# Optimization experiments

Hardware: AMD Instinct MI355X
Metric: run time of the kernel (lower is better)

Reference implementation:

```python
import jax, jax.numpy as jnp
import numpy as np

N_QUBITS = 10
N_LAYERS = 4
BATCH = 4096


def _apply_1q_batched(state, gate, q):
    # state: [B, 2,2,...,2]; gate: [B, 2, 2] (per-sample angles)
    s = jnp.moveaxis(state, 1 + q, -1)
    s = jnp.einsum('b...i,bji->b...j', s, gate)
    return jnp.moveaxis(s, -1, 1 + q)


def _apply_1q(state, gate, q):
    # gate: [2, 2] shared across batch
    s = jnp.moveaxis(state, 1 + q, -1)
    s = jnp.einsum('b...i,ji->b...j', s, gate)
    return jnp.moveaxis(s, -1, 1 + q)


def _apply_cnot(state, c, t):
    # bring control axis to 1 and target axis to 2, flip target where control==1
    s = jnp.moveaxis(state, (1 + c, 1 + t), (1, 2))
    s = jnp.concatenate([s[:, :1], s[:, 1:, ::-1]], axis=1)
    return jnp.moveaxis(s, (1, 2), (1 + c, 1 + t))


def _ry_rz_gate(theta_y, theta_z):
    # RZ(theta_z) @ RY(theta_y), both scalars -> [2, 2] complex
    hy = theta_y * 0.5
    cy, sy = jnp.cos(hy), jnp.sin(hy)
    ry = jnp.stack([jnp.stack([cy, -sy]), jnp.stack([sy, cy])]).astype(jnp.complex64)
    hz = theta_z * 0.5
    ph = jnp.exp(1j * jnp.stack([-hz, hz]).astype(jnp.complex64))  # diag of RZ
    return ph[:, None] * ry


def setup_inputs() -> dict:
    key = jax.random.key(0)
    kx, kp = jax.random.split(key)
    x = jax.random.uniform(kx, (BATCH, N_QUBITS), dtype=jnp.float32,
                           minval=-np.pi, maxval=np.pi)
    params = 0.5 * jax.random.normal(kp, (N_LAYERS, 2 * N_QUBITS), dtype=jnp.float32)
    return {"x": x, "params": params}


def reference(x, params):
    B, n = x.shape
    L = params.shape[0]
    dim = 2 ** n
    # |0...0> for every sample
    state = jnp.zeros((B, dim), jnp.complex64).at[:, 0].set(1.0)
    state = state.reshape((B,) + (2,) * n)

    # data encoding: RY(x[b, q]) on qubit q, per-sample angles
    half = x * 0.5
    c, s = jnp.cos(half), jnp.sin(half)  # [B, n]
    for q in range(n):
        g = jnp.stack([jnp.stack([c[:, q], -s[:, q]], -1),
                       jnp.stack([s[:, q], c[:, q]], -1)], -2).astype(jnp.complex64)  # [B,2,2]
        state = _apply_1q_batched(state, g, q)

    # variational layers: RY then RZ (fused) per qubit, then CNOT ring
    for l in range(L):
        for q in range(n):
            state = _apply_1q(state, _ry_rz_gate(params[l, q], params[l, n + q]), q)
        for q in range(n):
            state = _apply_cnot(state, q, (q + 1) % n)

    # <Z_q> = sum over basis states of |amp|^2 * (+1 if bit_q==0 else -1)
    probs = jnp.abs(state.reshape(B, dim)) ** 2  # float32 [B, 2^n]
    idx = jnp.arange(dim)
    bits = (idx[None, :] >> (n - 1 - jnp.arange(n))[:, None]) & 1  # [n, 2^n]
    signs = (1.0 - 2.0 * bits).astype(probs.dtype)
    return jnp.einsum('bs,qs->bq', probs, signs)  # [B, n]
```

## Files before the change

### kernel.cpp

```cpp
#include <hip/hip_runtime.h>

#define NQ 10

#if __has_builtin(__builtin_amdgcn_permlane16_swap)
#define HAVE_PLSWAP 1
#endif

template<int M>
__device__ __forceinline__ float lx(float v) {
    if constexpr (M == 1)
        return __int_as_float(__builtin_amdgcn_mov_dpp(__float_as_int(v), 0xB1, 0xF, 0xF, true));
    else if constexpr (M == 2)
        return __int_as_float(__builtin_amdgcn_mov_dpp(__float_as_int(v), 0x4E, 0xF, 0xF, true));
    else if constexpr (M == 8)
        return __int_as_float(__builtin_amdgcn_mov_dpp(__float_as_int(v), 0x128, 0xF, 0xF, true));
    else if constexpr (M == 4 || M == 16)
        return __int_as_float(__builtin_amdgcn_ds_swizzle(__float_as_int(v), (M << 10) | 0x1F));
    else
        return __shfl_xor(v, M, 64);
}

template<int M>
__device__ __forceinline__ float2 lx2(float2 v) {
    return make_float2(lx<M>(v.x), lx<M>(v.y));
}

template<int M>
__device__ __forceinline__ void xch(float& a, float& b) {
#ifdef HAVE_PLSWAP
    if constexpr (M == 16) {
        auto r1 = __builtin_amdgcn_permlane16_swap(__float_as_uint(a), __float_as_uint(b), false, false);
        auto r2 = __builtin_amdgcn_permlane16_swap(r1[1], r1[0], false, false);
        a = __uint_as_float(r2[0]);
        b = __uint_as_float(r2[1]);
    } else {
        auto r1 = __builtin_amdgcn_permlane32_swap(__float_as_uint(a), __float_as_uint(b), false, false);
        auto r2 = __builtin_amdgcn_permlane32_swap(r1[1], r1[0], false, false);
        a = __uint_as_float(r2[0]);
        b = __uint_as_float(r2[1]);
    }
#else
    a = lx<M>(a);
    b = lx<M>(b);
#endif
}

__device__ __forceinline__ float2 cmul(float2 a, float2 b) {
    return make_float2(a.x * b.x - a.y * b.y, a.x * b.y + a.y * b.x);
}

__device__ __forceinline__ float2 bperm2(int addr, float2 v) {
    float2 r;
    r.x = __int_as_float(__builtin_amdgcn_ds_bpermute(addr, __float_as_int(v.x)));
    r.y = __int_as_float(__builtin_amdgcn_ds_bpermute(addr, __float_as_int(v.y)));
    return r;
}

template<int M>
__device__ __forceinline__ void ry_lane(float2 st[16], int lane, float c, float s) {
    const float cB = (lane & M) ? s : -s;
#pragma unroll
    for (int r = 0; r < 16; ++r) {
        float2 part = lx2<M>(st[r]);
        st[r].x = c * st[r].x + cB * part.x;
        st[r].y = c * st[r].y + cB * part.y;
    }
}

template<int M>
__device__ __forceinline__ void ry_lane_x(float2 st[16], int lane, float c, float s) {
    const float cB = (lane & M) ? s : -s;
#pragma unroll
    for (int r = 0; r < 16; r += 2) {
        float pax = st[r].x, pay = st[r].y, pbx = st[r + 1].x, pby = st[r + 1].y;
        xch<M>(pax, pbx);
        xch<M>(pay, pby);
        st[r].x     = c * st[r].x     + cB * pax;
        st[r].y     = c * st[r].y     + cB * pay;
        st[r + 1].x = c * st[r + 1].x + cB * pbx;
        st[r + 1].y = c * st[r + 1].y + cB * pby;
    }
}

template<int M>
__device__ __forceinline__ void ry_lane_r(float sr[16], int lane, float c, float s) {
    const float cB = (lane & M) ? s : -s;
#pragma unroll
    for (int r = 0; r < 16; ++r) {
        float part = lx<M>(sr[r]);
        sr[r] = c * sr[r] + cB * part;
    }
}

template<int M>
__device__ __forceinline__ void ry_lane_r_x(float sr[16], int lane, float c, float s) {
    const float cB = (lane & M) ? s : -s;
#pragma unroll
    for (int r = 0; r < 16; r += 2) {
        float pa = sr[r], pb = sr[r + 1];
        xch<M>(pa, pb);
        sr[r]     = c * sr[r]     + cB * pa;
        sr[r + 1] = c * sr[r + 1] + cB * pb;
    }
}

template<int RB>
__device__ __forceinline__ void ry_reg_r(float sr[16], float c, float s) {
#pragma unroll
    for (int r = 0; r < 16; ++r) {
        if (r & RB) continue;
        float a0 = sr[r], a1 = sr[r | RB];
        sr[r]      = c * a0 - s * a1;
        sr[r | RB] = s * a0 + c * a1;
    }
}

template<int RB>
__device__ __forceinline__ void ry_reg(float2 st[16], float c, float s) {
#pragma unroll
    for (int r = 0; r < 16; ++r) {
        if (r & RB) continue;
        float2 a0 = st[r], a1 = st[r | RB];
        st[r].x = c * a0.x - s * a1.x;
        st[r].y = c * a0.y - s * a1.y;
        st[r | RB].x = s * a0.x + c * a1.x;
        st[r | RB].y = s * a0.y + c * a1.y;
    }
}

template<int MC, int RB>
__device__ __forceinline__ void cnot_lane_reg(float2 st[16], int lane) {
    const bool sel = (lane & MC) != 0;
#pragma unroll
    for (int r = 0; r < 16; ++r) {
        if (r & RB) continue;
        float2 lo = st[r], hi = st[r | RB];
        st[r]      = sel ? hi : lo;
        st[r | RB] = sel ? lo : hi;
    }
}

template<int RC, int RT>
__device__ __forceinline__ void cnot_reg_reg(float2 st[16]) {
#pragma unroll
    for (int r = 0; r < 16; ++r) {
        if ((r & RC) && !(r & RT)) {
            float2 t = st[r];
            st[r] = st[r | RT];
            st[r | RT] = t;
        }
    }
}

__device__ __forceinline__ void cnot_q9_q0(float2 st[16]) {
#pragma unroll
    for (int i = 0; i < 4; ++i) {
        const int ra = 4 * i + 1, rb = 4 * i + 3;
        xch<32>(st[ra].x, st[rb].x);
        xch<32>(st[ra].y, st[rb].y);
    }
}

__device__ __forceinline__ float wht64(float v, int lane) {
    float t;
    t = lx<1>(v);  v = (lane & 1)  ? (t - v) : (v + t);
    t = lx<2>(v);  v = (lane & 2)  ? (t - v) : (v + t);
    t = lx<4>(v);  v = (lane & 4)  ? (t - v) : (v + t);
    t = lx<8>(v);  v = (lane & 8)  ? (t - v) : (v + t);
    t = lx<16>(v); v = (lane & 16) ? (t - v) : (v + t);
    t = lx<32>(v); v = (lane & 32) ? (t - v) : (v + t);
    return v;
}

__global__ __launch_bounds__(256)
void pqc_kernel(const float* __restrict__ x,
                const float* __restrict__ params,
                float* __restrict__ out, int B) {
    const int lane = threadIdx.x & 63;
    const int wave = threadIdx.x >> 6;
    const int b = blockIdx.x * 4 + wave;
    if (b >= B) return;

    const float* xb = x + (long)b * NQ;
    float c0,s0,c1,s1,c2,s2,c3,s3,c4,s4,c5,s5,c6,s6,c7,s7,c8,s8,c9,s9;
    __sincosf(0.5f * xb[0], &s0, &c0);
    __sincosf(0.5f * xb[1], &s1, &c1);
    __sincosf(0.5f * xb[2], &s2, &c2);
    __sincosf(0.5f * xb[3], &s3, &c3);
    __sincosf(0.5f * xb[4], &s4, &c4);
    __sincosf(0.5f * xb[5], &s5, &c5);
    __sincosf(0.5f * xb[6], &s6, &c6);
    __sincosf(0.5f * xb[7], &s7, &c7);
    __sincosf(0.5f * xb[8], &s8, &c8);
    __sincosf(0.5f * xb[9], &s9, &c9);
    float laneprod = ((lane & 32) ? s0 : c0) * ((lane & 16) ? s1 : c1)
                   * ((lane & 8)  ? s2 : c2) * ((lane & 4)  ? s3 : c3)
                   * ((lane & 2)  ? s4 : c4) * ((lane & 1)  ? s5 : c5);
    float Ar[4] = { c6 * c7, c6 * s7, s6 * c7, s6 * s7 };
    float Br[4] = { c8 * c9, c8 * s9, s8 * c9, s8 * s9 };
    Ar[0] *= laneprod; Ar[1] *= laneprod; Ar[2] *= laneprod; Ar[3] *= laneprod;

    float sr[16];
#pragma unroll
    for (int r = 0; r < 16; ++r) sr[r] = Ar[r >> 2] * Br[r & 3];

    const float* p0 = params;
    float c, s;
    __sincosf(0.5f * p0[0], &s, &c); ry_lane_r_x<32>(sr, lane, c, s);
    __sincosf(0.5f * p0[1], &s, &c); ry_lane_r_x<16>(sr, lane, c, s);
    __sincosf(0.5f * p0[2], &s, &c); ry_lane_r<8>(sr, lane, c, s);
    __sincosf(0.5f * p0[3], &s, &c); ry_lane_r<4>(sr, lane, c, s);
    __sincosf(0.5f * p0[4], &s, &c); ry_lane_r<2>(sr, lane, c, s);
    __sincosf(0.5f * p0[5], &s, &c); ry_lane_r<1>(sr, lane, c, s);
    __sincosf(0.5f * p0[6], &s, &c); ry_reg_r<8>(sr, c, s);
    __sincosf(0.5f * p0[7], &s, &c); ry_reg_r<4>(sr, c, s);
    __sincosf(0.5f * p0[8], &s, &c); ry_reg_r<2>(sr, c, s);
    __sincosf(0.5f * p0[9], &s, &c); ry_reg_r<1>(sr, c, s);

    float2 st[16];
    {
        float sz, cz;
        __sincosf(0.5f * p0[10], &sz, &cz);
        float2 PL = make_float2(cz, (lane & 32) ? sz : -sz);
        __sincosf(0.5f * p0[11], &sz, &cz);
        PL = cmul(PL, make_float2(cz, (lane & 16) ? sz : -sz));
        __sincosf(0.5f * p0[12], &sz, &cz);
        PL = cmul(PL, make_float2(cz, (lane & 8) ? sz : -sz));
        __sincosf(0.5f * p0[13], &sz, &cz);
        PL = cmul(PL, make_float2(cz, (lane & 4) ? sz : -sz));
        __sincosf(0.5f * p0[14], &sz, &cz);
        PL = cmul(PL, make_float2(cz, (lane & 2) ? sz : -sz));
        __sincosf(0.5f * p0[15], &sz, &cz);
        PL = cmul(PL, make_float2(cz, (lane & 1) ? sz : -sz));

        float z6s, z6c, z7s, z7c, z8s, z8c, z9s, z9c;
        __sincosf(0.5f * p0[16], &z6s, &z6c);
        __sincosf(0.5f * p0[17], &z7s, &z7c);
        __sincosf(0.5f * p0[18], &z8s, &z8c);
        __sincosf(0.5f * p0[19], &z9s, &z9c);
        float2 A[4], Bb[4];
        A[0] = cmul(make_float2(z6c, -z6s), make_float2(z7c, -z7s));
        A[1] = cmul(make_float2(z6c, -z6s), make_float2(z7c,  z7s));
        A[2] = cmul(make_float2(z6c,  z6s), make_float2(z7c, -z7s));
        A[3] = cmul(make_float2(z6c,  z6s), make_float2(z7c,  z7s));
        Bb[0] = cmul(make_float2(z8c, -z8s), make_float2(z9c, -z9s));
        Bb[1] = cmul(make_float2(z8c, -z8s), make_float2(z9c,  z9s));
        Bb[2] = cmul(make_float2(z8c,  z8s), make_float2(z9c, -z9s));
        Bb[3] = cmul(make_float2(z8c,  z8s), make_float2(z9c,  z9s));
        A[0] = cmul(A[0], PL); A[1] = cmul(A[1], PL);
        A[2] = cmul(A[2], PL); A[3] = cmul(A[3], PL);
#pragma unroll
        for (int r = 0; r < 16; ++r) {
            float2 t = make_float2(sr[r] * A[r >> 2].x, sr[r] * A[r >> 2].y);
            st[r] = cmul(t, Bb[r & 3]);
        }
    }

    {
        const int addr = ((lane ^ (lane >> 1)) & 63) << 2;
#pragma unroll
        for (int r = 0; r < 16; ++r) st[r] = bperm2(addr, st[r]);
        cnot_lane_reg<1, 8>(st, lane);
        cnot_reg_reg<8, 4>(st);
        cnot_reg_reg<4, 2>(st);
        cnot_reg_reg<2, 1>(st);
        cnot_q9_q0(st);
    }

#pragma unroll
    for (int l = 1; l < 4; ++l) {
        const float* pl = params + l * 2 * NQ;

        __sincosf(0.5f * pl[0], &s, &c); ry_lane_x<32>(st, lane, c, s);
        __sincosf(0.5f * pl[1], &s, &c); ry_lane_x<16>(st, lane, c, s);
        __sincosf(0.5f * pl[2], &s, &c); ry_lane<8>(st, lane, c, s);
        __sincosf(0.5f * pl[3], &s, &c); ry_lane<4>(st, lane, c, s);
        __sincosf(0.5f * pl[4], &s, &c); ry_lane<2>(st, lane, c, s);
        __sincosf(0.5f * pl[5], &s, &c); ry_lane<1>(st, lane, c, s);
        __sincosf(0.5f * pl[6], &s, &c); ry_reg<8>(st, c, s);
        __sincosf(0.5f * pl[7], &s, &c); ry_reg<4>(st, c, s);
        __sincosf(0.5f * pl[8], &s, &c); ry_reg<2>(st, c, s);
        __sincosf(0.5f * pl[9], &s, &c); ry_reg<1>(st, c, s);

        if (l < 3) {
            float sz, cz;
            __sincosf(0.5f * pl[10], &sz, &cz);
            float2 PL = make_float2(cz, (lane & 32) ? sz : -sz);
            __sincosf(0.5f * pl[11], &sz, &cz);
            PL = cmul(PL, make_float2(cz, (lane & 16) ? sz : -sz));
            __sincosf(0.5f * pl[12], &sz, &cz);
            PL = cmul(PL, make_float2(cz, (lane & 8) ? sz : -sz));
            __sincosf(0.5f * pl[13], &sz, &cz);
            PL = cmul(PL, make_float2(cz, (lane & 4) ? sz : -sz));
            __sincosf(0.5f * pl[14], &sz, &cz);
            PL = cmul(PL, make_float2(cz, (lane & 2) ? sz : -sz));
            __sincosf(0.5f * pl[15], &sz, &cz);
            PL = cmul(PL, make_float2(cz, (lane & 1) ? sz : -sz));

            float z6s, z6c, z7s, z7c, z8s, z8c, z9s, z9c;
            __sincosf(0.5f * pl[16], &z6s, &z6c);
            __sincosf(0.5f * pl[17], &z7s, &z7c);
            __sincosf(0.5f * pl[18], &z8s, &z8c);
            __sincosf(0.5f * pl[19], &z9s, &z9c);
            float2 A[4], Bb[4];
            A[0] = cmul(make_float2(z6c, -z6s), make_float2(z7c, -z7s));
            A[1] = cmul(make_float2(z6c, -z6s), make_float2(z7c,  z7s));
            A[2] = cmul(make_float2(z6c,  z6s), make_float2(z7c, -z7s));
            A[3] = cmul(make_float2(z6c,  z6s), make_float2(z7c,  z7s));
            Bb[0] = cmul(make_float2(z8c, -z8s), make_float2(z9c, -z9s));
            Bb[1] = cmul(make_float2(z8c, -z8s), make_float2(z9c,  z9s));
            Bb[2] = cmul(make_float2(z8c,  z8s), make_float2(z9c, -z9s));
            Bb[3] = cmul(make_float2(z8c,  z8s), make_float2(z9c,  z9s));
            A[0] = cmul(A[0], PL); A[1] = cmul(A[1], PL);
            A[2] = cmul(A[2], PL); A[3] = cmul(A[3], PL);
#pragma unroll
            for (int r = 0; r < 16; ++r)
                st[r] = cmul(cmul(st[r], A[r >> 2]), Bb[r & 3]);

            const int addr = ((lane ^ (lane >> 1)) & 63) << 2;
#pragma unroll
            for (int r = 0; r < 16; ++r) st[r] = bperm2(addr, st[r]);
            cnot_lane_reg<1, 8>(st, lane);
            cnot_reg_reg<8, 4>(st);
            cnot_reg_reg<4, 2>(st);
            cnot_reg_reg<2, 1>(st);
            cnot_q9_q0(st);
        }
    }

    float lane_sum = 0.f, A3 = 0.f, A32 = 0.f, A321 = 0.f, A3210 = 0.f;
#pragma unroll
    for (int r = 0; r < 16; ++r) {
        float p = st[r].x * st[r].x + st[r].y * st[r].y;
        const int p3 = (r >> 3) & 1;
        const int p32 = p3 ^ ((r >> 2) & 1);
        const int p321 = p32 ^ ((r >> 1) & 1);
        const int p3210 = p321 ^ (r & 1);
        lane_sum += p;
        A3    += p3    ? -p : p;
        A32   += p32   ? -p : p;
        A321  += p321  ? -p : p;
        A3210 += p3210 ? -p : p;
    }
    const float wLS   = wht64(lane_sum, lane);
    const float w3    = wht64(A3, lane);
    const float w32   = wht64(A32, lane);
    const float w321  = wht64(A321, lane);
    const float w3210 = wht64(A3210, lane);

    const long base = (long)b * NQ;
    if (lane == 31) out[base + 0] = w3210;
    if (lane == 48) out[base + 1] = wLS;
    if (lane == 56) out[base + 2] = wLS;
    if (lane == 60) out[base + 3] = wLS;
    if (lane == 62) out[base + 4] = wLS;
    if (lane == 63) {
        out[base + 5] = wLS;
        out[base + 6] = w3;
        out[base + 7] = w32;
        out[base + 8] = w321;
        out[base + 9] = w3210;
    }
}

extern "C" void kernel_launch(void* const* d_in, const int* in_sizes, int n_in,
                              void* d_out, int out_size, void* d_ws, size_t ws_size,
                              hipStream_t stream) {
    const float* x = (const float*)d_in[0];
    const float* params = (const float*)d_in[1];
    float* out = (float*)d_out;
    const int B = in_sizes[0] / NQ;
    const int grid = (B + 3) / 4;
    pqc_kernel<<<grid, 256, 0, stream>>>(x, params, out, B);
}
```

Before: 87.61 us.

## Precompute gate trig tables in a setup kernel and read them from workspace

Adds a setup kernel that computes sincos of the encoding angles per sample and all parameter gate cos/sin, per-lane folded RZ diagonals and Bb factors into the workspace. The main kernel then loads these instead of recomputing transcendental functions in every wave. It also swaps the lane-xor-4 exchange from ds_swizzle to a two-DPP sequence. The cost is an extra kernel launch plus global memory round trips, and the old path is kept as a fallback when no workspace is available.

```diff
diff --git a/kernel.cpp b/kernel.cpp
--- a/kernel.cpp
+++ b/kernel.cpp
@@ -5,6 +5,11 @@
 #if __has_builtin(__builtin_amdgcn_permlane16_swap)
 #define HAVE_PLSWAP 1
 #endif
+
+constexpr int GATE_OFF = 0;
+constexpr int BB_OFF = 80;
+constexpr int AFOLD_OFF = 112;
+constexpr int ENC_OFF = 2048;
 
 template<int M>
 __device__ __forceinline__ float lx(float v) {
@@ -12,10 +17,13 @@
         return __int_as_float(__builtin_amdgcn_mov_dpp(__float_as_int(v), 0xB1, 0xF, 0xF, true));
     else if constexpr (M == 2)
         return __int_as_float(__builtin_amdgcn_mov_dpp(__float_as_int(v), 0x4E, 0xF, 0xF, true));
-    else if constexpr (M == 8)
+    else if constexpr (M == 4) {
+        int t = __builtin_amdgcn_mov_dpp(__float_as_int(v), 0x141, 0xF, 0xF, true);
+        return __int_as_float(__builtin_amdgcn_mov_dpp(t, 0x1B, 0xF, 0xF, true));
+    } else if constexpr (M == 8)
         return __int_as_float(__builtin_amdgcn_mov_dpp(__float_as_int(v), 0x128, 0xF, 0xF, true));
-    else if constexpr (M == 4 || M == 16)
-        return __int_as_float(__builtin_amdgcn_ds_swizzle(__float_as_int(v), (M << 10) | 0x1F));
+    else if constexpr (M == 16)
+        return __int_as_float(__builtin_amdgcn_ds_swizzle(__float_as_int(v), (16 << 10) | 0x1F));
     else
         return __shfl_xor(v, M, 64);
 }
@@ -173,116 +181,25 @@
 }
 
 __global__ __launch_bounds__(256)
-void pqc_kernel(const float* __restrict__ x,
-                const float* __restrict__ params,
-                float* __restrict__ out, int B) {
-    const int lane = threadIdx.x & 63;
-    const int wave = threadIdx.x >> 6;
-    const int b = blockIdx.x * 4 + wave;
-    if (b >= B) return;
-
-    const float* xb = x + (long)b * NQ;
-    float c0,s0,c1,s1,c2,s2,c3,s3,c4,s4,c5,s5,c6,s6,c7,s7,c8,s8,c9,s9;
-    __sincosf(0.5f * xb[0], &s0, &c0);
-    __sincosf(0.5f * xb[1], &s1, &c1);
-    __sincosf(0.5f * xb[2], &s2, &c2);
-    __sincosf(0.5f * xb[3], &s3, &c3);
-    __sincosf(0.5f * xb[4], &s4, &c4);
-    __sincosf(0.5f * xb[5], &s5, &c5);
-    __sincosf(0.5f * xb[6], &s6, &c6);
-    __sincosf(0.5f * xb[7], &s7, &c7);
-    __sincosf(0.5f * xb[8], &s8, &c8);
-    __sincosf(0.5f * xb[9], &s9, &c9);
-    float laneprod = ((lane & 32) ? s0 : c0) * ((lane & 16) ? s1 : c1)
-                   * ((lane & 8)  ? s2 : c2) * ((lane & 4)  ? s3 : c3)
-                   * ((lane & 2)  ? s4 : c4) * ((lane & 1)  ? s5 : c5);
-    float Ar[4] = { c6 * c7, c6 * s7, s6 * c7, s6 * s7 };
-    float Br[4] = { c8 * c9, c8 * s9, s8 * c9, s8 * s9 };
-    Ar[0] *= laneprod; Ar[1] *= laneprod; Ar[2] *= laneprod; Ar[3] *= laneprod;
-
-    float sr[16];
-#pragma unroll
-    for (int r = 0; r < 16; ++r) sr[r] = Ar[r >> 2] * Br[r & 3];
-
-    const float* p0 = params;
-    float c, s;
-    __sincosf(0.5f * p0[0], &s, &c); ry_lane_r_x<32>(sr, lane, c, s);
-    __sincosf(0.5f * p0[1], &s, &c); ry_lane_r_x<16>(sr, lane, c, s);
-    __sincosf(0.5f * p0[2], &s, &c); ry_lane_r<8>(sr, lane, c, s);
-    __sincosf(0.5f * p0[3], &s, &c); ry_lane_r<4>(sr, lane, c, s);
-    __sincosf(0.5f * p0[4], &s, &c); ry_lane_r<2>(sr, lane, c, s);
-    __sincosf(0.5f * p0[5], &s, &c); ry_lane_r<1>(sr, lane, c, s);
-    __sincosf(0.5f * p0[6], &s, &c); ry_reg_r<8>(sr, c, s);
-    __sincosf(0.5f * p0[7], &s, &c); ry_reg_r<4>(sr, c, s);
-    __sincosf(0.5f * p0[8], &s, &c); ry_reg_r<2>(sr, c, s);
-    __sincosf(0.5f * p0[9], &s, &c); ry_reg_r<1>(sr, c, s);
-
-    float2 st[16];
-    {
-        float sz, cz;
-        __sincosf(0.5f * p0[10], &sz, &cz);
-        float2 PL = make_float2(cz, (lane & 32) ? sz : -sz);
-        __sincosf(0.5f * p0[11], &sz, &cz);
-        PL = cmul(PL, make_float2(cz, (lane & 16) ? sz : -sz));
-        __sincosf(0.5f * p0[12], &sz, &cz);
-        PL = cmul(PL, make_float2(cz, (lane & 8) ? sz : -sz));
-        __sincosf(0.5f * p0[13], &sz, &cz);
-        PL = cmul(PL, make_float2(cz, (lane & 4) ? sz : -sz));
-        __sincosf(0.5f * p0[14], &sz, &cz);
-        PL = cmul(PL, make_float2(cz, (lane & 2) ? sz : -sz));
-        __sincosf(0.5f * p0[15], &sz, &cz);
-        PL = cmul(PL, make_float2(cz, (lane & 1) ? sz : -sz));
-
-        float z6s, z6c, z7s, z7c, z8s, z8c, z9s, z9c;
-        __sincosf(0.5f * p0[16], &z6s, &z6c);
-        __sincosf(0.5f * p0[17], &z7s, &z7c);
-        __sincosf(0.5f * p0[18], &z8s, &z8c);
-        __sincosf(0.5f * p0[19], &z9s, &z9c);
-        float2 A[4], Bb[4];
-        A[0] = cmul(make_float2(z6c, -z6s), make_float2(z7c, -z7s));
-        A[1] = cmul(make_float2(z6c, -z6s), make_float2(z7c,  z7s));
-        A[2] = cmul(make_float2(z6c,  z6s), make_float2(z7c, -z7s));
-        A[3] = cmul(make_float2(z6c,  z6s), make_float2(z7c,  z7s));
-        Bb[0] = cmul(make_float2(z8c, -z8s), make_float2(z9c, -z9s));
-        Bb[1] = cmul(make_float2(z8c, -z8s), make_float2(z9c,  z9s));
-        Bb[2] = cmul(make_float2(z8c,  z8s), make_float2(z9c, -z9s));
-        Bb[3] = cmul(make_float2(z8c,  z8s), make_float2(z9c,  z9s));
-        A[0] = cmul(A[0], PL); A[1] = cmul(A[1], PL);
-        A[2] = cmul(A[2], PL); A[3] = cmul(A[3], PL);
-#pragma unroll
-        for (int r = 0; r < 16; ++r) {
-            float2 t = make_float2(sr[r] * A[r >> 2].x, sr[r] * A[r >> 2].y);
-            st[r] = cmul(t, Bb[r & 3]);
-        }
-    }
-
-    {
-        const int addr = ((lane ^ (lane >> 1)) & 63) << 2;
-#pragma unroll
-        for (int r = 0; r < 16; ++r) st[r] = bperm2(addr, st[r]);
-        cnot_lane_reg<1, 8>(st, lane);
-        cnot_reg_reg<8, 4>(st);
-        cnot_reg_reg<4, 2>(st);
-        cnot_reg_reg<2, 1>(st);
-        cnot_q9_q0(st);
-    }
-
-#pragma unroll
-    for (int l = 1; l < 4; ++l) {
-        const float* pl = params + l * 2 * NQ;
-
-        __sincosf(0.5f * pl[0], &s, &c); ry_lane_x<32>(st, lane, c, s);
-        __sincosf(0.5f * pl[1], &s, &c); ry_lane_x<16>(st, lane, c, s);
-        __sincosf(0.5f * pl[2], &s, &c); ry_lane<8>(st, lane, c, s);
-        __sincosf(0.5f * pl[3], &s, &c); ry_lane<4>(st, lane, c, s);
-        __sincosf(0.5f * pl[4], &s, &c); ry_lane<2>(st, lane, c, s);
-        __sincosf(0.5f * pl[5], &s, &c); ry_lane<1>(st, lane, c, s);
-        __sincosf(0.5f * pl[6], &s, &c); ry_reg<8>(st, c, s);
-        __sincosf(0.5f * pl[7], &s, &c); ry_reg<4>(st, c, s);
-        __sincosf(0.5f * pl[8], &s, &c); ry_reg<2>(st, c, s);
-        __sincosf(0.5f * pl[9], &s, &c); ry_reg<1>(st, c, s);
-
-        if (l < 3) {
+void setup_kernel(const float* __restrict__ x, const float* __restrict__ params,
+                  float* __restrict__ ws, int B) {
+    const int t = threadIdx.x;
+    const int g = blockIdx.x * 256 + t;
+    if (g < B) {
+        const float* xg = x + (long)g * NQ;
+        float* e = ws + ENC_OFF + g * 2 * NQ;
+#pragma unroll
+        for (int q = 0; q < NQ; ++q) {
+            float s, c;
+            __sincosf(0.5f * xg[q], &s, &c);
+            e[2 * q] = c;
+            e[2 * q + 1] = s;
+        }
+    }
+    if (blockIdx.x == 0) {
+        if (t < 192) {
+            const int l = t >> 6, lane = t & 63;
+            const float* pl = params + l * 2 * NQ;
             float sz, cz;
             __sincosf(0.5f * pl[10], &sz, &cz);
             float2 PL = make_float2(cz, (lane & 32) ? sz : -sz);
@@ -296,23 +213,182 @@
             PL = cmul(PL, make_float2(cz, (lane & 2) ? sz : -sz));
             __sincosf(0.5f * pl[15], &sz, &cz);
             PL = cmul(PL, make_float2(cz, (lane & 1) ? sz : -sz));
-
+            float s6, c6, s7, c7;
+            __sincosf(0.5f * pl[16], &s6, &c6);
+            __sincosf(0.5f * pl[17], &s7, &c7);
+            float* dst = ws + AFOLD_OFF + (l * 64 + lane) * 8;
+#pragma unroll
+            for (int k = 0; k < 4; ++k) {
+                float2 A = cmul(make_float2(c6, (k & 2) ? s6 : -s6),
+                                make_float2(c7, (k & 1) ? s7 : -s7));
+                A = cmul(A, PL);
+                dst[2 * k] = A.x;
+                dst[2 * k + 1] = A.y;
+            }
+        } else if (t < 232) {
+            const int i = t - 192;
+            float s, c;
+            __sincosf(0.5f * params[(i / 10) * 2 * NQ + (i % 10)], &s, &c);
+            ws[GATE_OFF + i * 2] = c;
+            ws[GATE_OFF + i * 2 + 1] = s;
+        } else if (t < 244) {
+            const int i = t - 232;
+            const int l = i >> 2, k = i & 3;
+            const float* pl = params + l * 2 * NQ;
+            float s8, c8, s9, c9;
+            __sincosf(0.5f * pl[18], &s8, &c8);
+            __sincosf(0.5f * pl[19], &s9, &c9);
+            float2 v = cmul(make_float2(c8, (k & 2) ? s8 : -s8),
+                            make_float2(c9, (k & 1) ? s9 : -s9));
+            ws[BB_OFF + i * 2] = v.x;
+            ws[BB_OFF + i * 2 + 1] = v.y;
+        }
+    }
+}
+
+template<bool WS>
+__global__ __launch_bounds__(256)
+void pqc_kernel(const float* __restrict__ x,
+                const float* __restrict__ params,
+                const float* __restrict__ ws,
+                float* __restrict__ out, int B) {
+    const int lane = threadIdx.x & 63;
+    const int wave = threadIdx.x >> 6;
+    const int b = blockIdx.x * 4 + wave;
+    if (b >= B) return;
+
+    float c0,s0,c1,s1,c2,s2,c3,s3,c4,s4,c5,s5,c6,s6,c7,s7,c8,s8,c9,s9;
+    if constexpr (WS) {
+        const int sb = __builtin_amdgcn_readfirstlane(b);
+        const float* e = ws + ENC_OFF + sb * 2 * NQ;
+        c0 = e[0];  s0 = e[1];  c1 = e[2];  s1 = e[3];
+        c2 = e[4];  s2 = e[5];  c3 = e[6];  s3 = e[7];
+        c4 = e[8];  s4 = e[9];  c5 = e[10]; s5 = e[11];
+        c6 = e[12]; s6 = e[13]; c7 = e[14]; s7 = e[15];
+        c8 = e[16]; s8 = e[17]; c9 = e[18]; s9 = e[19];
+    } else {
+        const float* xb = x + (long)b * NQ;
+        __sincosf(0.5f * xb[0], &s0, &c0);
+        __sincosf(0.5f * xb[1], &s1, &c1);
+        __sincosf(0.5f * xb[2], &s2, &c2);
+        __sincosf(0.5f * xb[3], &s3, &c3);
+        __sincosf(0.5f * xb[4], &s4, &c4);
+        __sincosf(0.5f * xb[5], &s5, &c5);
+        __sincosf(0.5f * xb[6], &s6, &c6);
+        __sincosf(0.5f * xb[7], &s7, &c7);
+        __sincosf(0.5f * xb[8], &s8, &c8);
+        __sincosf(0.5f * xb[9], &s9, &c9);
+    }
+    float laneprod = ((lane & 32) ? s0 : c0) * ((lane & 16) ? s1 : c1)
+                   * ((lane & 8)  ? s2 : c2) * ((lane & 4)  ? s3 : c3)
+                   * ((lane & 2)  ? s4 : c4) * ((lane & 1)  ? s5 : c5);
+    float Ar[4] = { c6 * c7, c6 * s7, s6 * c7, s6 * s7 };
+    float Br[4] = { c8 * c9, c8 * s9, s8 * c9, s8 * s9 };
+    Ar[0] *= laneprod; Ar[1] *= laneprod; Ar[2] *= laneprod; Ar[3] *= laneprod;
+
+    float sr[16];
+#pragma unroll
+    for (int r = 0; r < 16; ++r) sr[r] = Ar[r >> 2] * Br[r & 3];
+
+    auto gate_cs = [&](int l, int q, float& c, float& s) {
+        if constexpr (WS) {
+            c = ws[GATE_OFF + (l * 10 + q) * 2];
+            s = ws[GATE_OFF + (l * 10 + q) * 2 + 1];
+        } else {
+            __sincosf(0.5f * params[l * 2 * NQ + q], &s, &c);
+        }
+    };
+
+    float2 A[4], Bb[4];
+    auto load_diag = [&](int l) {
+        if constexpr (WS) {
+            const float4* af = (const float4*)(ws + AFOLD_OFF) + (l * 64 + lane) * 2;
+            float4 a01 = af[0], a23 = af[1];
+            A[0] = make_float2(a01.x, a01.y);
+            A[1] = make_float2(a01.z, a01.w);
+            A[2] = make_float2(a23.x, a23.y);
+            A[3] = make_float2(a23.z, a23.w);
+            const float* bb = ws + BB_OFF + l * 8;
+            Bb[0] = make_float2(bb[0], bb[1]);
+            Bb[1] = make_float2(bb[2], bb[3]);
+            Bb[2] = make_float2(bb[4], bb[5]);
+            Bb[3] = make_float2(bb[6], bb[7]);
+        } else {
+            const float* pl = params + l * 2 * NQ;
+            float sz, cz;
+            __sincosf(0.5f * pl[10], &sz, &cz);
+            float2 PL = make_float2(cz, (lane & 32) ? sz : -sz);
+            __sincosf(0.5f * pl[11], &sz, &cz);
+            PL = cmul(PL, make_float2(cz, (lane & 16) ? sz : -sz));
+            __sincosf(0.5f * pl[12], &sz, &cz);
+            PL = cmul(PL, make_float2(cz, (lane & 8) ? sz : -sz));
+            __sincosf(0.5f * pl[13], &sz, &cz);
+            PL = cmul(PL, make_float2(cz, (lane & 4) ? sz : -sz));
+            __sincosf(0.5f * pl[14], &sz, &cz);
+            PL = cmul(PL, make_float2(cz, (lane & 2) ? sz : -sz));
+            __sincosf(0.5f * pl[15], &sz, &cz);
+            PL = cmul(PL, make_float2(cz, (lane & 1) ? sz : -sz));
             float z6s, z6c, z7s, z7c, z8s, z8c, z9s, z9c;
             __sincosf(0.5f * pl[16], &z6s, &z6c);
             __sincosf(0.5f * pl[17], &z7s, &z7c);
             __sincosf(0.5f * pl[18], &z8s, &z8c);
             __sincosf(0.5f * pl[19], &z9s, &z9c);
-            float2 A[4], Bb[4];
-            A[0] = cmul(make_float2(z6c, -z6s), make_float2(z7c, -z7s));
-            A[1] = cmul(make_float2(z6c, -z6s), make_float2(z7c,  z7s));
-            A[2] = cmul(make_float2(z6c,  z6s), make_float2(z7c, -z7s));
-            A[3] = cmul(make_float2(z6c,  z6s), make_float2(z7c,  z7s));
-            Bb[0] = cmul(make_float2(z8c, -z8s), make_float2(z9c, -z9s));
-            Bb[1] = cmul(make_float2(z8c, -z8s), make_float2(z9c,  z9s));
-            Bb[2] = cmul(make_float2(z8c,  z8s), make_float2(z9c, -z9s));
-            Bb[3] = cmul(make_float2(z8c,  z8s), make_float2(z9c,  z9s));
-            A[0] = cmul(A[0], PL); A[1] = cmul(A[1], PL);
-            A[2] = cmul(A[2], PL); A[3] = cmul(A[3], PL);
+#pragma unroll
+            for (int k = 0; k < 4; ++k) {
+                A[k] = cmul(cmul(make_float2(z6c, (k & 2) ? z6s : -z6s),
+                                 make_float2(z7c, (k & 1) ? z7s : -z7s)), PL);
+                Bb[k] = cmul(make_float2(z8c, (k & 2) ? z8s : -z8s),
+                             make_float2(z9c, (k & 1) ? z9s : -z9s));
+            }
+        }
+    };
+
+    float c, s;
+    gate_cs(0, 0, c, s); ry_lane_r_x<32>(sr, lane, c, s);
+    gate_cs(0, 1, c, s); ry_lane_r_x<16>(sr, lane, c, s);
+    gate_cs(0, 2, c, s); ry_lane_r<8>(sr, lane, c, s);
+    gate_cs(0, 3, c, s); ry_lane_r<4>(sr, lane, c, s);
+    gate_cs(0, 4, c, s); ry_lane_r<2>(sr, lane, c, s);
+    gate_cs(0, 5, c, s); ry_lane_r<1>(sr, lane, c, s);
+    gate_cs(0, 6, c, s); ry_reg_r<8>(sr, c, s);
+    gate_cs(0, 7, c, s); ry_reg_r<4>(sr, c, s);
+    gate_cs(0, 8, c, s); ry_reg_r<2>(sr, c, s);
+    gate_cs(0, 9, c, s); ry_reg_r<1>(sr, c, s);
+
+    float2 st[16];
+    load_diag(0);
+#pragma unroll
+    for (int r = 0; r < 16; ++r) {
+        float2 t = make_float2(sr[r] * A[r >> 2].x, sr[r] * A[r >> 2].y);
+        st[r] = cmul(t, Bb[r & 3]);
+    }
+
+    {
+        const int addr = ((lane ^ (lane >> 1)) & 63) << 2;
+#pragma unroll
+        for (int r = 0; r < 16; ++r) st[r] = bperm2(addr, st[r]);
+        cnot_lane_reg<1, 8>(st, lane);
+        cnot_reg_reg<8, 4>(st);
+        cnot_reg_reg<4, 2>(st);
+        cnot_reg_reg<2, 1>(st);
+        cnot_q9_q0(st);
+    }
+
+#pragma unroll
+    for (int l = 1; l < 4; ++l) {
+        gate_cs(l, 0, c, s); ry_lane_x<32>(st, lane, c, s);
+        gate_cs(l, 1, c, s); ry_lane_x<16>(st, lane, c, s);
+        gate_cs(l, 2, c, s); ry_lane<8>(st, lane, c, s);
+        gate_cs(l, 3, c, s); ry_lane<4>(st, lane, c, s);
+        gate_cs(l, 4, c, s); ry_lane<2>(st, lane, c, s);
+        gate_cs(l, 5, c, s); ry_lane<1>(st, lane, c, s);
+        gate_cs(l, 6, c, s); ry_reg<8>(st, c, s);
+        gate_cs(l, 7, c, s); ry_reg<4>(st, c, s);
+        gate_cs(l, 8, c, s); ry_reg<2>(st, c, s);
+        gate_cs(l, 9, c, s); ry_reg<1>(st, c, s);
+
+        if (l < 3) {
+            load_diag(l);
 #pragma unroll
             for (int r = 0; r < 16; ++r)
                 st[r] = cmul(cmul(st[r], A[r >> 2]), Bb[r & 3]);
@@ -371,5 +447,13 @@
     float* out = (float*)d_out;
     const int B = in_sizes[0] / NQ;
     const int grid = (B + 3) / 4;
-    pqc_kernel<<<grid, 256, 0, stream>>>(x, params, out, B);
-}
+
+    const size_t needed = (size_t)(ENC_OFF + B * 2 * NQ) * sizeof(float);
+    if (d_ws != nullptr && ws_size >= needed) {
+        float* ws = (float*)d_ws;
+        setup_kernel<<<(B + 255) / 256, 256, 0, stream>>>(x, params, ws, B);
+        pqc_kernel<true><<<grid, 256, 0, stream>>>(x, params, ws, out, B);
+    } else {
+        pqc_kernel<false><<<grid, 256, 0, stream>>>(x, params, nullptr, out, B);
+    }
+}
```

New measurement: 84.20 us. -3.9%, faster.

## Fold encoding RY and first-layer RY angles into one product state

Applied to the files above, without the earlier changes.

Merges the per-sample RY(x) encoding with the first layer's RY(params) by adding the angles, since both rotate about Y on the same qubit. The first-layer RZ is then absorbed analytically, so the state before the first CNOT ring is a closed-form product state. This removes the ten lane/register rotation passes of layer 0 and their cross-lane shuffles. It also replaces the ds_swizzle for xor-4 lane exchange with two DPP moves, and compacts the phase-table construction into a loop without changing the math.

```diff
diff --git a/kernel.cpp b/kernel.cpp
--- a/kernel.cpp
+++ b/kernel.cpp
@@ -12,10 +12,13 @@
         return __int_as_float(__builtin_amdgcn_mov_dpp(__float_as_int(v), 0xB1, 0xF, 0xF, true));
     else if constexpr (M == 2)
         return __int_as_float(__builtin_amdgcn_mov_dpp(__float_as_int(v), 0x4E, 0xF, 0xF, true));
-    else if constexpr (M == 8)
+    else if constexpr (M == 4) {
+        int t = __builtin_amdgcn_mov_dpp(__float_as_int(v), 0x141, 0xF, 0xF, true);
+        return __int_as_float(__builtin_amdgcn_mov_dpp(t, 0x1B, 0xF, 0xF, true));
+    } else if constexpr (M == 8)
         return __int_as_float(__builtin_amdgcn_mov_dpp(__float_as_int(v), 0x128, 0xF, 0xF, true));
-    else if constexpr (M == 4 || M == 16)
-        return __int_as_float(__builtin_amdgcn_ds_swizzle(__float_as_int(v), (M << 10) | 0x1F));
+    else if constexpr (M == 16)
+        return __int_as_float(__builtin_amdgcn_ds_swizzle(__float_as_int(v), (16 << 10) | 0x1F));
     else
         return __shfl_xor(v, M, 64);
 }
@@ -82,39 +85,6 @@
     }
 }
 
-template<int M>
-__device__ __forceinline__ void ry_lane_r(float sr[16], int lane, float c, float s) {
-    const float cB = (lane & M) ? s : -s;
-#pragma unroll
-    for (int r = 0; r < 16; ++r) {
-        float part = lx<M>(sr[r]);
-        sr[r] = c * sr[r] + cB * part;
-    }
-}
-
-template<int M>
-__device__ __forceinline__ void ry_lane_r_x(float sr[16], int lane, float c, float s) {
-    const float cB = (lane & M) ? s : -s;
-#pragma unroll
-    for (int r = 0; r < 16; r += 2) {
-        float pa = sr[r], pb = sr[r + 1];
-        xch<M>(pa, pb);
-        sr[r]     = c * sr[r]     + cB * pa;
-        sr[r + 1] = c * sr[r + 1] + cB * pb;
-    }
-}
-
-template<int RB>
-__device__ __forceinline__ void ry_reg_r(float sr[16], float c, float s) {
-#pragma unroll
-    for (int r = 0; r < 16; ++r) {
-        if (r & RB) continue;
-        float a0 = sr[r], a1 = sr[r | RB];
-        sr[r]      = c * a0 - s * a1;
-        sr[r | RB] = s * a0 + c * a1;
-    }
-}
-
 template<int RB>
 __device__ __forceinline__ void ry_reg(float2 st[16], float c, float s) {
 #pragma unroll
@@ -182,79 +152,53 @@
     if (b >= B) return;
 
     const float* xb = x + (long)b * NQ;
-    float c0,s0,c1,s1,c2,s2,c3,s3,c4,s4,c5,s5,c6,s6,c7,s7,c8,s8,c9,s9;
-    __sincosf(0.5f * xb[0], &s0, &c0);
-    __sincosf(0.5f * xb[1], &s1, &c1);
-    __sincosf(0.5f * xb[2], &s2, &c2);
-    __sincosf(0.5f * xb[3], &s3, &c3);
-    __sincosf(0.5f * xb[4], &s4, &c4);
-    __sincosf(0.5f * xb[5], &s5, &c5);
-    __sincosf(0.5f * xb[6], &s6, &c6);
-    __sincosf(0.5f * xb[7], &s7, &c7);
-    __sincosf(0.5f * xb[8], &s8, &c8);
-    __sincosf(0.5f * xb[9], &s9, &c9);
-    float laneprod = ((lane & 32) ? s0 : c0) * ((lane & 16) ? s1 : c1)
-                   * ((lane & 8)  ? s2 : c2) * ((lane & 4)  ? s3 : c3)
-                   * ((lane & 2)  ? s4 : c4) * ((lane & 1)  ? s5 : c5);
-    float Ar[4] = { c6 * c7, c6 * s7, s6 * c7, s6 * s7 };
-    float Br[4] = { c8 * c9, c8 * s9, s8 * c9, s8 * s9 };
-    Ar[0] *= laneprod; Ar[1] *= laneprod; Ar[2] *= laneprod; Ar[3] *= laneprod;
-
-    float sr[16];
-#pragma unroll
-    for (int r = 0; r < 16; ++r) sr[r] = Ar[r >> 2] * Br[r & 3];
-
     const float* p0 = params;
-    float c, s;
-    __sincosf(0.5f * p0[0], &s, &c); ry_lane_r_x<32>(sr, lane, c, s);
-    __sincosf(0.5f * p0[1], &s, &c); ry_lane_r_x<16>(sr, lane, c, s);
-    __sincosf(0.5f * p0[2], &s, &c); ry_lane_r<8>(sr, lane, c, s);
-    __sincosf(0.5f * p0[3], &s, &c); ry_lane_r<4>(sr, lane, c, s);
-    __sincosf(0.5f * p0[4], &s, &c); ry_lane_r<2>(sr, lane, c, s);
-    __sincosf(0.5f * p0[5], &s, &c); ry_lane_r<1>(sr, lane, c, s);
-    __sincosf(0.5f * p0[6], &s, &c); ry_reg_r<8>(sr, c, s);
-    __sincosf(0.5f * p0[7], &s, &c); ry_reg_r<4>(sr, c, s);
-    __sincosf(0.5f * p0[8], &s, &c); ry_reg_r<2>(sr, c, s);
-    __sincosf(0.5f * p0[9], &s, &c); ry_reg_r<1>(sr, c, s);
+    float a0,b0,a1,b1,a2,b2,a3,b3,a4,b4,a5,b5,a6,b6,a7,b7,a8,b8,a9,b9;
+    float cz0,sz0,cz1,sz1,cz2,sz2,cz3,sz3,cz4,sz4,cz5,sz5,cz6,sz6,cz7,sz7,cz8,sz8,cz9,sz9;
+    __sincosf(0.5f * (xb[0] + p0[0]), &b0, &a0);
+    __sincosf(0.5f * (xb[1] + p0[1]), &b1, &a1);
+    __sincosf(0.5f * (xb[2] + p0[2]), &b2, &a2);
+    __sincosf(0.5f * (xb[3] + p0[3]), &b3, &a3);
+    __sincosf(0.5f * (xb[4] + p0[4]), &b4, &a4);
+    __sincosf(0.5f * (xb[5] + p0[5]), &b5, &a5);
+    __sincosf(0.5f * (xb[6] + p0[6]), &b6, &a6);
+    __sincosf(0.5f * (xb[7] + p0[7]), &b7, &a7);
+    __sincosf(0.5f * (xb[8] + p0[8]), &b8, &a8);
+    __sincosf(0.5f * (xb[9] + p0[9]), &b9, &a9);
+    __sincosf(0.5f * p0[10], &sz0, &cz0);
+    __sincosf(0.5f * p0[11], &sz1, &cz1);
+    __sincosf(0.5f * p0[12], &sz2, &cz2);
+    __sincosf(0.5f * p0[13], &sz3, &cz3);
+    __sincosf(0.5f * p0[14], &sz4, &cz4);
+    __sincosf(0.5f * p0[15], &sz5, &cz5);
+    __sincosf(0.5f * p0[16], &sz6, &cz6);
+    __sincosf(0.5f * p0[17], &sz7, &cz7);
+    __sincosf(0.5f * p0[18], &sz8, &cz8);
+    __sincosf(0.5f * p0[19], &sz9, &cz9);
+
+    float R = ((lane & 32) ? b0 : a0) * ((lane & 16) ? b1 : a1)
+            * ((lane & 8)  ? b2 : a2) * ((lane & 4)  ? b3 : a3)
+            * ((lane & 2)  ? b4 : a4) * ((lane & 1)  ? b5 : a5);
+    float2 P = make_float2(cz0, (lane & 32) ? sz0 : -sz0);
+    P = cmul(P, make_float2(cz1, (lane & 16) ? sz1 : -sz1));
+    P = cmul(P, make_float2(cz2, (lane & 8)  ? sz2 : -sz2));
+    P = cmul(P, make_float2(cz3, (lane & 4)  ? sz3 : -sz3));
+    P = cmul(P, make_float2(cz4, (lane & 2)  ? sz4 : -sz4));
+    P = cmul(P, make_float2(cz5, (lane & 1)  ? sz5 : -sz5));
+    float2 laneC = make_float2(R * P.x, R * P.y);
+
+    float2 u6l = make_float2(a6 * cz6, -a6 * sz6), u6h = make_float2(b6 * cz6, b6 * sz6);
+    float2 u7l = make_float2(a7 * cz7, -a7 * sz7), u7h = make_float2(b7 * cz7, b7 * sz7);
+    float2 u8l = make_float2(a8 * cz8, -a8 * sz8), u8h = make_float2(b8 * cz8, b8 * sz8);
+    float2 u9l = make_float2(a9 * cz9, -a9 * sz9), u9h = make_float2(b9 * cz9, b9 * sz9);
+    float2 A2[4] = { cmul(u6l, u7l), cmul(u6l, u7h), cmul(u6h, u7l), cmul(u6h, u7h) };
+    float2 B2[4] = { cmul(u8l, u9l), cmul(u8l, u9h), cmul(u8h, u9l), cmul(u8h, u9h) };
+    float2 LA[4] = { cmul(laneC, A2[0]), cmul(laneC, A2[1]),
+                     cmul(laneC, A2[2]), cmul(laneC, A2[3]) };
 
     float2 st[16];
-    {
-        float sz, cz;
-        __sincosf(0.5f * p0[10], &sz, &cz);
-        float2 PL = make_float2(cz, (lane & 32) ? sz : -sz);
-        __sincosf(0.5f * p0[11], &sz, &cz);
-        PL = cmul(PL, make_float2(cz, (lane & 16) ? sz : -sz));
-        __sincosf(0.5f * p0[12], &sz, &cz);
-        PL = cmul(PL, make_float2(cz, (lane & 8) ? sz : -sz));
-        __sincosf(0.5f * p0[13], &sz, &cz);
-        PL = cmul(PL, make_float2(cz, (lane & 4) ? sz : -sz));
-        __sincosf(0.5f * p0[14], &sz, &cz);
-        PL = cmul(PL, make_float2(cz, (lane & 2) ? sz : -sz));
-        __sincosf(0.5f * p0[15], &sz, &cz);
-        PL = cmul(PL, make_float2(cz, (lane & 1) ? sz : -sz));
-
-        float z6s, z6c, z7s, z7c, z8s, z8c, z9s, z9c;
-        __sincosf(0.5f * p0[16], &z6s, &z6c);
-        __sincosf(0.5f * p0[17], &z7s, &z7c);
-        __sincosf(0.5f * p0[18], &z8s, &z8c);
-        __sincosf(0.5f * p0[19], &z9s, &z9c);
-        float2 A[4], Bb[4];
-        A[0] = cmul(make_float2(z6c, -z6s), make_float2(z7c, -z7s));
-        A[1] = cmul(make_float2(z6c, -z6s), make_float2(z7c,  z7s));
-        A[2] = cmul(make_float2(z6c,  z6s), make_float2(z7c, -z7s));
-        A[3] = cmul(make_float2(z6c,  z6s), make_float2(z7c,  z7s));
-        Bb[0] = cmul(make_float2(z8c, -z8s), make_float2(z9c, -z9s));
-        Bb[1] = cmul(make_float2(z8c, -z8s), make_float2(z9c,  z9s));
-        Bb[2] = cmul(make_float2(z8c,  z8s), make_float2(z9c, -z9s));
-        Bb[3] = cmul(make_float2(z8c,  z8s), make_float2(z9c,  z9s));
-        A[0] = cmul(A[0], PL); A[1] = cmul(A[1], PL);
-        A[2] = cmul(A[2], PL); A[3] = cmul(A[3], PL);
-#pragma unroll
-        for (int r = 0; r < 16; ++r) {
-            float2 t = make_float2(sr[r] * A[r >> 2].x, sr[r] * A[r >> 2].y);
-            st[r] = cmul(t, Bb[r & 3]);
-        }
-    }
+#pragma unroll
+    for (int r = 0; r < 16; ++r) st[r] = cmul(LA[r >> 2], B2[r & 3]);
 
     {
         const int addr = ((lane ^ (lane >> 1)) & 63) << 2;
@@ -267,6 +211,7 @@
         cnot_q9_q0(st);
     }
 
+    float c, s;
 #pragma unroll
     for (int l = 1; l < 4; ++l) {
         const float* pl = params + l * 2 * NQ;
@@ -303,16 +248,13 @@
             __sincosf(0.5f * pl[18], &z8s, &z8c);
             __sincosf(0.5f * pl[19], &z9s, &z9c);
             float2 A[4], Bb[4];
-            A[0] = cmul(make_float2(z6c, -z6s), make_float2(z7c, -z7s));
-            A[1] = cmul(make_float2(z6c, -z6s), make_float2(z7c,  z7s));
-            A[2] = cmul(make_float2(z6c,  z6s), make_float2(z7c, -z7s));
-            A[3] = cmul(make_float2(z6c,  z6s), make_float2(z7c,  z7s));
-            Bb[0] = cmul(make_float2(z8c, -z8s), make_float2(z9c, -z9s));
-            Bb[1] = cmul(make_float2(z8c, -z8s), make_float2(z9c,  z9s));
-            Bb[2] = cmul(make_float2(z8c,  z8s), make_float2(z9c, -z9s));
-            Bb[3] = cmul(make_float2(z8c,  z8s), make_float2(z9c,  z9s));
-            A[0] = cmul(A[0], PL); A[1] = cmul(A[1], PL);
-            A[2] = cmul(A[2], PL); A[3] = cmul(A[3], PL);
+#pragma unroll
+            for (int k = 0; k < 4; ++k) {
+                A[k] = cmul(cmul(make_float2(z6c, (k & 2) ? z6s : -z6s),
+                                 make_float2(z7c, (k & 1) ? z7s : -z7s)), PL);
+                Bb[k] = cmul(make_float2(z8c, (k & 2) ? z8s : -z8s),
+                             make_float2(z9c, (k & 1) ? z9s : -z9s));
+            }
 #pragma unroll
             for (int r = 0; r < 16; ++r)
                 st[r] = cmul(cmul(st[r], A[r >> 2]), Bb[r & 3]);
```

Result: faster. 82.81 us (-5.5%).
